# Optimization experiments

Measured on AMD Instinct MI355X. Metric: run time of the kernel, lower is better.

## Reference

```python
import jax, jax.numpy as jnp
import numpy as np

B, T, I, H, O = 8192, 128, 28, 64, 10


def setup_inputs() -> dict:
    key = jax.random.key(0)
    ks = jax.random.split(key, 7)
    s_ih = 1.0 / np.sqrt(H)
    return {
        "x": jax.random.normal(ks[0], (B, T, I), dtype=jnp.float32),
        "W_ih": jax.random.uniform(ks[1], (H, I), minval=-s_ih, maxval=s_ih, dtype=jnp.float32),
        "W_hh": jax.random.uniform(ks[2], (H, H), minval=-s_ih, maxval=s_ih, dtype=jnp.float32),
        "b_ih": jax.random.uniform(ks[3], (H,), minval=-s_ih, maxval=s_ih, dtype=jnp.float32),
        "b_hh": jax.random.uniform(ks[4], (H,), minval=-s_ih, maxval=s_ih, dtype=jnp.float32),
        "W_out": jax.random.uniform(ks[5], (O, H), minval=-1.0 / np.sqrt(H), maxval=1.0 / np.sqrt(H), dtype=jnp.float32),
        "b_out": jax.random.uniform(ks[6], (O,), minval=-1.0 / np.sqrt(H), maxval=1.0 / np.sqrt(H), dtype=jnp.float32),
    }


def reference(x, W_ih, W_hh, b_ih, b_hh, W_out, b_out):
    # Elman RNN: h_t = tanh(x_t @ W_ih^T + b_ih + h_{t-1} @ W_hh^T + b_hh)
    # Precompute the input projection for all timesteps in one big GEMM.
    xproj = jnp.einsum('bti,hi->bth', x, W_ih) + b_ih + b_hh  # [B,T,H]
    h0 = jnp.zeros((x.shape[0], W_hh.shape[0]), dtype=x.dtype)

    def step(h, xp_t):
        h_new = jnp.tanh(xp_t + h @ W_hh.T)
        return h_new, None

    # scan over time axis: move T to leading axis
    h_last, _ = jax.lax.scan(step, h0, jnp.swapaxes(xproj, 0, 1))
    # final linear on last hidden state (r_out[:, -1, :])
    return h_last @ W_out.T + b_out  # [B,O]
```

## Files before the change

### kernel.cpp

```cpp
#include <hip/hip_runtime.h>

#define B_ 8192
#define T_ 128
#define I_ 28
#define H_ 64
#define O_ 10
#define RING 8
#define SLOTF 512
#define HS 72

typedef __attribute__((ext_vector_type(8))) short bf16x8;
typedef __attribute__((ext_vector_type(4))) float f32x4;
typedef __attribute__((ext_vector_type(4))) unsigned int u32x4;

__device__ __forceinline__ unsigned short f2bf(float f) {
    unsigned int u = __builtin_bit_cast(unsigned int, f);
    u += 0x7fffu + ((u >> 16) & 1u);
    return (unsigned short)(u >> 16);
}
__device__ __forceinline__ unsigned int cvtpk(float lo, float hi) {
    unsigned int r;
    asm("v_cvt_pk_bf16_f32 %0, %1, %2" : "=v"(r) : "v"(lo), "v"(hi));
    return r;
}
__device__ __forceinline__ bf16x8 mkfrag(unsigned int a, unsigned int b,
                                         unsigned int c, unsigned int d) {
    u32x4 u = {a, b, c, d};
    return __builtin_bit_cast(bf16x8, u);
}
__device__ __forceinline__ float exp2f_fast(float x) {
#if __has_builtin(__builtin_amdgcn_exp2f)
    return __builtin_amdgcn_exp2f(x);
#else
    return __expf(x * 0.6931471805599453f);
#endif
}
__device__ __forceinline__ unsigned int tanh2_bf(float xa, float xb) {
    float ta = exp2f_fast(xa * 2.885390081777927f);
    float tb = exp2f_fast(xb * 2.885390081777927f);
    float ra = __builtin_amdgcn_rcpf(1.0f + ta);
    float rb = __builtin_amdgcn_rcpf(1.0f + tb);
    return cvtpk(fmaf(-2.0f, ra, 1.0f), fmaf(-2.0f, rb, 1.0f));
}

__device__ __forceinline__ void gload_lds(const float* g, float* l) {
    __builtin_amdgcn_global_load_lds(
        (const __attribute__((address_space(1))) unsigned int*)g,
        (__attribute__((address_space(3))) unsigned int*)l, 16, 0, 0);
}

#define MFMA(A, B, C) __builtin_amdgcn_mfma_f32_16x16x32_bf16((A), (B), (C), 0, 0, 0)

__launch_bounds__(256, 1)
__global__ void rnn_split_kernel(const float* __restrict__ x,
                                 const float* __restrict__ W_ih,
                                 const float* __restrict__ W_hh,
                                 const float* __restrict__ b_ih,
                                 const float* __restrict__ b_hh,
                                 const float* __restrict__ W_out,
                                 const float* __restrict__ b_out,
                                 float* __restrict__ out) {
    __shared__ __align__(16) float xs[RING][SLOTF];
    __shared__ __align__(16) unsigned short hb[2][16 * HS];

    const int tid = threadIdx.x;
    const int lane = tid & 63;
    const int w = tid >> 6;
    const int m = lane & 15;
    const int g = lane >> 4;
    const int b0 = blockIdx.x * 16;
    const int row = b0 + m;

    bf16x8 wih, whhA, whhB;
    f32x4 biasC;
    {
        const int nA = 8 * (m >> 2) + 4 * (w & 1) + (m & 3) + 32 * (w >> 1);
#pragma unroll
        for (int j = 0; j < 8; ++j) {
            const int k = 8 * g + j;
            wih[j]  = (k < I_) ? (short)f2bf(W_ih[nA * I_ + k]) : (short)0;
            whhA[j] = (short)f2bf(W_hh[nA * H_ + k]);
            whhB[j] = (short)f2bf(W_hh[nA * H_ + 32 + k]);
        }
#pragma unroll
        for (int r = 0; r < 4; ++r) {
            const int nb = 8 * g + 4 * (w & 1) + r + 32 * (w >> 1);
            biasC[r] = b_ih[nb] + b_hh[nb];
        }
    }
    const int wbase = m * HS + 8 * g + 4 * (w & 1) + 32 * (w >> 1);
    const int rbase = m * HS + 8 * g;

    const int cA = lane;
    const int cB = (64 + lane <= 111) ? (64 + lane) : 111;
    const float* gA = x + (size_t)(b0 + cA / 7) * (T_ * I_) + (cA % 7) * 4;
    const float* gB = x + (size_t)(b0 + cB / 7) * (T_ * I_) + (cB % 7) * 4;

#define ISSUE(s, tt) do {                                                    \
        const int tc_ = ((tt) < T_) ? (tt) : (T_ - 1);                       \
        gload_lds(gA + (size_t)tc_ * I_, &xs[s][0]);                         \
        gload_lds(gB + (size_t)tc_ * I_, &xs[s][256]);                       \
    } while (0)

    const int xoff = m * 28 + g * 8;
    const int hoff = (g < 3) ? 4 : 0;

#define XFRAG(s, dst) do {                                                   \
        const f32x4 lo_ = *reinterpret_cast<const f32x4*>(&xs[s][xoff]);     \
        const f32x4 hi_ = *reinterpret_cast<const f32x4*>(&xs[s][xoff + hoff]); \
        dst = mkfrag(cvtpk(lo_[0], lo_[1]), cvtpk(lo_[2], lo_[3]),           \
                     cvtpk(hi_[0], hi_[1]), cvtpk(hi_[2], hi_[3]));          \
    } while (0)

    __builtin_amdgcn_sched_barrier(0);
    asm volatile("s_waitcnt vmcnt(0)" ::: "memory");
    __builtin_amdgcn_sched_barrier(0);

    if (w == 0) {
        ISSUE(0, 0); ISSUE(1, 1); ISSUE(2, 2); ISSUE(3, 3);
        ISSUE(4, 4); ISSUE(5, 5); ISSUE(6, 6); ISSUE(7, 7);
        asm volatile("s_waitcnt vmcnt(10)" ::: "memory");
    }
    asm volatile("s_barrier" ::: "memory");

    f32x4 pxA, pxB;
    {
        bf16x8 xf0; XFRAG(0, xf0);
        pxA = MFMA(wih, xf0, biasC);
    }
    bf16x8 h0f = mkfrag(0, 0, 0, 0), h1f = mkfrag(0, 0, 0, 0);

#define STEP(u, TB, PXC, PXN) do {                                            \
        bf16x8 xf; XFRAG(((u) + 1) & 7, xf);                                  \
        PXN = MFMA(wih, xf, biasC);                                           \
        f32x4 aA = MFMA(whhA, h0f, PXC);                                      \
        aA = MFMA(whhB, h1f, aA);                                             \
        const unsigned int p0 = tanh2_bf(aA[0], aA[1]);                       \
        const unsigned int p1 = tanh2_bf(aA[2], aA[3]);                       \
        uint2 pv; pv.x = p0; pv.y = p1;                                       \
        *reinterpret_cast<uint2*>(&hb[((u) + 1) & 1][wbase]) = pv;            \
        if (w == 0) {                                                         \
            ISSUE((u), (TB) + (u) + 8);                                       \
            asm volatile("s_waitcnt vmcnt(10)" ::: "memory");                 \
        }                                                                     \
        asm volatile("s_waitcnt lgkmcnt(0)\n\ts_barrier" ::: "memory");       \
        h0f = *reinterpret_cast<const bf16x8*>(&hb[((u) + 1) & 1][rbase]);    \
        h1f = *reinterpret_cast<const bf16x8*>(&hb[((u) + 1) & 1][rbase + 32]); \
    } while (0)

    for (int tb = 0; tb < T_; tb += 8) {
        STEP(0, tb, pxA, pxB); STEP(1, tb, pxB, pxA);
        STEP(2, tb, pxA, pxB); STEP(3, tb, pxB, pxA);
        STEP(4, tb, pxA, pxB); STEP(5, tb, pxB, pxA);
        STEP(6, tb, pxA, pxB); STEP(7, tb, pxB, pxA);
    }
#undef STEP
#undef XFRAG
#undef ISSUE

    if (w == 0) {
        float hf[16];
        {
            u32x4 H0 = __builtin_bit_cast(u32x4, h0f);
            u32x4 H1 = __builtin_bit_cast(u32x4, h1f);
#pragma unroll
            for (int p = 0; p < 4; ++p) {
                hf[2 * p]     = __builtin_bit_cast(float, H0[p] << 16);
                hf[2 * p + 1] = __builtin_bit_cast(float, H0[p] & 0xffff0000u);
                hf[8 + 2 * p]     = __builtin_bit_cast(float, H1[p] << 16);
                hf[8 + 2 * p + 1] = __builtin_bit_cast(float, H1[p] & 0xffff0000u);
            }
        }
        float pacc[O_];
#pragma unroll
        for (int o = 0; o < O_; ++o) {
            const float* wo = W_out + o * H_;
            float4 wA = *reinterpret_cast<const float4*>(wo + 8 * g);
            float4 wB = *reinterpret_cast<const float4*>(wo + 8 * g + 4);
            float4 wC = *reinterpret_cast<const float4*>(wo + 32 + 8 * g);
            float4 wD = *reinterpret_cast<const float4*>(wo + 32 + 8 * g + 4);
            float s = hf[0] * wA.x + hf[1] * wA.y + hf[2] * wA.z + hf[3] * wA.w
                    + hf[4] * wB.x + hf[5] * wB.y + hf[6] * wB.z + hf[7] * wB.w
                    + hf[8] * wC.x + hf[9] * wC.y + hf[10] * wC.z + hf[11] * wC.w
                    + hf[12] * wD.x + hf[13] * wD.y + hf[14] * wD.z + hf[15] * wD.w;
            s += __shfl_xor(s, 16);
            s += __shfl_xor(s, 32);
            pacc[o] = s;
        }
        if (g == 0) {
#pragma unroll
            for (int o = 0; o < O_; ++o)
                out[(size_t)row * O_ + o] = pacc[o] + b_out[o];
        }
    }
}

extern "C" void kernel_launch(void* const* d_in, const int* in_sizes, int n_in,
                              void* d_out, int out_size, void* d_ws, size_t ws_size,
                              hipStream_t stream) {
    const float* x     = (const float*)d_in[0];
    const float* W_ih  = (const float*)d_in[1];
    const float* W_hh  = (const float*)d_in[2];
    const float* b_ih  = (const float*)d_in[3];
    const float* b_hh  = (const float*)d_in[4];
    const float* W_out = (const float*)d_in[5];
    const float* b_out = (const float*)d_in[6];
    float* out = (float*)d_out;

    dim3 grid(B_ / 16);
    dim3 block(256);
    rnn_split_kernel<<<grid, block, 0, stream>>>(x, W_ih, W_hh, b_ih, b_hh,
                                                 W_out, b_out, out);
}
```

Before: 44.86 us.

## Replace LDS ring of async x loads with per-wave register prefetch

Drops the shared-memory ring that wave 0 filled with global_load_lds, and has every wave load its own x fragment straight from global memory into registers, prefetched four timesteps ahead in rotating register sets. This removes the LDS staging traffic, wave 0's extra issue work and the vmcnt waits inside the barrier-synchronised step. In exchange each of the four waves now loads the same x data redundantly, which multiplies global/L2 request traffic, and load latency must be hidden by the four-step register lookahead rather than the eight-slot ring.

```diff
diff --git a/kernel.cpp b/kernel.cpp
--- a/kernel.cpp
+++ b/kernel.cpp
@@ -5,8 +5,6 @@
 #define I_ 28
 #define H_ 64
 #define O_ 10
-#define RING 8
-#define SLOTF 512
 #define HS 72
 
 typedef __attribute__((ext_vector_type(8))) short bf16x8;
@@ -43,12 +41,6 @@
     return cvtpk(fmaf(-2.0f, ra, 1.0f), fmaf(-2.0f, rb, 1.0f));
 }
 
-__device__ __forceinline__ void gload_lds(const float* g, float* l) {
-    __builtin_amdgcn_global_load_lds(
-        (const __attribute__((address_space(1))) unsigned int*)g,
-        (__attribute__((address_space(3))) unsigned int*)l, 16, 0, 0);
-}
-
 #define MFMA(A, B, C) __builtin_amdgcn_mfma_f32_16x16x32_bf16((A), (B), (C), 0, 0, 0)
 
 __launch_bounds__(256, 1)
@@ -60,7 +52,6 @@
                                  const float* __restrict__ W_out,
                                  const float* __restrict__ b_out,
                                  float* __restrict__ out) {
-    __shared__ __align__(16) float xs[RING][SLOTF];
     __shared__ __align__(16) unsigned short hb[2][16 * HS];
 
     const int tid = threadIdx.x;
@@ -91,72 +82,56 @@
     const int wbase = m * HS + 8 * g + 4 * (w & 1) + 32 * (w >> 1);
     const int rbase = m * HS + 8 * g;
 
-    const int cA = lane;
-    const int cB = (64 + lane <= 111) ? (64 + lane) : 111;
-    const float* gA = x + (size_t)(b0 + cA / 7) * (T_ * I_) + (cA % 7) * 4;
-    const float* gB = x + (size_t)(b0 + cB / 7) * (T_ * I_) + (cB % 7) * 4;
+    const float* xp  = x + (size_t)row * (T_ * I_) + 8 * g;
+    const float* xph = (g < 3) ? (xp + 4) : xp;
 
-#define ISSUE(s, tt) do {                                                    \
+    float4 l0, h0v, l1, h1v, l2, h2v, l3, h3v;
+
+#define LOADX(LO, HI, tt) do {                                               \
         const int tc_ = ((tt) < T_) ? (tt) : (T_ - 1);                       \
-        gload_lds(gA + (size_t)tc_ * I_, &xs[s][0]);                         \
-        gload_lds(gB + (size_t)tc_ * I_, &xs[s][256]);                       \
+        LO = *reinterpret_cast<const float4*>(xp + tc_ * I_);                \
+        HI = *reinterpret_cast<const float4*>(xph + tc_ * I_);               \
     } while (0)
 
-    const int xoff = m * 28 + g * 8;
-    const int hoff = (g < 3) ? 4 : 0;
+#define XF(LO, HI, dst)                                                      \
+    dst = mkfrag(cvtpk(LO.x, LO.y), cvtpk(LO.z, LO.w),                       \
+                 cvtpk(HI.x, HI.y), cvtpk(HI.z, HI.w))
 
-#define XFRAG(s, dst) do {                                                   \
-        const f32x4 lo_ = *reinterpret_cast<const f32x4*>(&xs[s][xoff]);     \
-        const f32x4 hi_ = *reinterpret_cast<const f32x4*>(&xs[s][xoff + hoff]); \
-        dst = mkfrag(cvtpk(lo_[0], lo_[1]), cvtpk(lo_[2], lo_[3]),           \
-                     cvtpk(hi_[0], hi_[1]), cvtpk(hi_[2], hi_[3]));          \
-    } while (0)
-
-    __builtin_amdgcn_sched_barrier(0);
-    asm volatile("s_waitcnt vmcnt(0)" ::: "memory");
-    __builtin_amdgcn_sched_barrier(0);
-
-    if (w == 0) {
-        ISSUE(0, 0); ISSUE(1, 1); ISSUE(2, 2); ISSUE(3, 3);
-        ISSUE(4, 4); ISSUE(5, 5); ISSUE(6, 6); ISSUE(7, 7);
-        asm volatile("s_waitcnt vmcnt(10)" ::: "memory");
-    }
-    asm volatile("s_barrier" ::: "memory");
-
+    LOADX(l0, h0v, 0);
     f32x4 pxA, pxB;
     {
-        bf16x8 xf0; XFRAG(0, xf0);
+        bf16x8 xf0; XF(l0, h0v, xf0);
         pxA = MFMA(wih, xf0, biasC);
     }
+    LOADX(l0, h0v, 4);
+    LOADX(l1, h1v, 1); LOADX(l2, h2v, 2); LOADX(l3, h3v, 3);
+
     bf16x8 h0f = mkfrag(0, 0, 0, 0), h1f = mkfrag(0, 0, 0, 0);
 
-#define STEP(u, TB, PXC, PXN) do {                                            \
-        bf16x8 xf; XFRAG(((u) + 1) & 7, xf);                                  \
+#define STEP(u, TB, PXC, PXN, LO, HI) do {                                    \
+        bf16x8 xf; XF(LO, HI, xf);                                            \
         PXN = MFMA(wih, xf, biasC);                                           \
+        LOADX(LO, HI, (TB) + (u) + 5);                                        \
         f32x4 aA = MFMA(whhA, h0f, PXC);                                      \
         aA = MFMA(whhB, h1f, aA);                                             \
         const unsigned int p0 = tanh2_bf(aA[0], aA[1]);                       \
         const unsigned int p1 = tanh2_bf(aA[2], aA[3]);                       \
         uint2 pv; pv.x = p0; pv.y = p1;                                       \
         *reinterpret_cast<uint2*>(&hb[((u) + 1) & 1][wbase]) = pv;            \
-        if (w == 0) {                                                         \
-            ISSUE((u), (TB) + (u) + 8);                                       \
-            asm volatile("s_waitcnt vmcnt(10)" ::: "memory");                 \
-        }                                                                     \
         asm volatile("s_waitcnt lgkmcnt(0)\n\ts_barrier" ::: "memory");       \
         h0f = *reinterpret_cast<const bf16x8*>(&hb[((u) + 1) & 1][rbase]);    \
         h1f = *reinterpret_cast<const bf16x8*>(&hb[((u) + 1) & 1][rbase + 32]); \
     } while (0)
 
     for (int tb = 0; tb < T_; tb += 8) {
-        STEP(0, tb, pxA, pxB); STEP(1, tb, pxB, pxA);
-        STEP(2, tb, pxA, pxB); STEP(3, tb, pxB, pxA);
-        STEP(4, tb, pxA, pxB); STEP(5, tb, pxB, pxA);
-        STEP(6, tb, pxA, pxB); STEP(7, tb, pxB, pxA);
+        STEP(0, tb, pxA, pxB, l1, h1v); STEP(1, tb, pxB, pxA, l2, h2v);
+        STEP(2, tb, pxA, pxB, l3, h3v); STEP(3, tb, pxB, pxA, l0, h0v);
+        STEP(4, tb, pxA, pxB, l1, h1v); STEP(5, tb, pxB, pxA, l2, h2v);
+        STEP(6, tb, pxA, pxB, l3, h3v); STEP(7, tb, pxB, pxA, l0, h0v);
     }
 #undef STEP
-#undef XFRAG
-#undef ISSUE
+#undef XF
+#undef LOADX
 
     if (w == 0) {
         float hf[16];
```

Result: slower. 68.39 us (+52.5%).

## Halve waves per block, each wave computing two hidden-unit tiles

Applied to the files above, without the earlier changes.

Each block now uses 2 waves instead of 4, with each wave holding weights for two 16-column hidden tiles and issuing twice the MFMA and tanh work per timestep. The hidden-state store becomes a single 16-byte write per lane. This reduces barrier participants and LDS write count per step but lengthens each wave's serial per-step critical path and lowers wave-level parallelism on the CU.

```diff
diff --git a/kernel.cpp b/kernel.cpp
--- a/kernel.cpp
+++ b/kernel.cpp
@@ -51,15 +51,15 @@
 
 #define MFMA(A, B, C) __builtin_amdgcn_mfma_f32_16x16x32_bf16((A), (B), (C), 0, 0, 0)
 
-__launch_bounds__(256, 1)
-__global__ void rnn_split_kernel(const float* __restrict__ x,
-                                 const float* __restrict__ W_ih,
-                                 const float* __restrict__ W_hh,
-                                 const float* __restrict__ b_ih,
-                                 const float* __restrict__ b_hh,
-                                 const float* __restrict__ W_out,
-                                 const float* __restrict__ b_out,
-                                 float* __restrict__ out) {
+__launch_bounds__(128, 1)
+__global__ void rnn_split2_kernel(const float* __restrict__ x,
+                                  const float* __restrict__ W_ih,
+                                  const float* __restrict__ W_hh,
+                                  const float* __restrict__ b_ih,
+                                  const float* __restrict__ b_hh,
+                                  const float* __restrict__ W_out,
+                                  const float* __restrict__ b_out,
+                                  float* __restrict__ out) {
     __shared__ __align__(16) float xs[RING][SLOTF];
     __shared__ __align__(16) unsigned short hb[2][16 * HS];
 
@@ -71,24 +71,30 @@
     const int b0 = blockIdx.x * 16;
     const int row = b0 + m;
 
-    bf16x8 wih, whhA, whhB;
-    f32x4 biasC;
-    {
-        const int nA = 8 * (m >> 2) + 4 * (w & 1) + (m & 3) + 32 * (w >> 1);
+    bf16x8 wih0, wih1, whhA0, whhA1, whhB0, whhB1;
+    f32x4 biasC0, biasC1;
+#pragma unroll
+    for (int tt = 0; tt < 2; ++tt) {
+        const int t = 2 * w + tt;
+        const int nA = 8 * (m >> 2) + 4 * (t & 1) + (m & 3) + 32 * (t >> 1);
+        bf16x8 wi, wa, wb;
 #pragma unroll
         for (int j = 0; j < 8; ++j) {
             const int k = 8 * g + j;
-            wih[j]  = (k < I_) ? (short)f2bf(W_ih[nA * I_ + k]) : (short)0;
-            whhA[j] = (short)f2bf(W_hh[nA * H_ + k]);
-            whhB[j] = (short)f2bf(W_hh[nA * H_ + 32 + k]);
-        }
+            wi[j] = (k < I_) ? (short)f2bf(W_ih[nA * I_ + k]) : (short)0;
+            wa[j] = (short)f2bf(W_hh[nA * H_ + k]);
+            wb[j] = (short)f2bf(W_hh[nA * H_ + 32 + k]);
+        }
+        f32x4 bc;
 #pragma unroll
         for (int r = 0; r < 4; ++r) {
-            const int nb = 8 * g + 4 * (w & 1) + r + 32 * (w >> 1);
-            biasC[r] = b_ih[nb] + b_hh[nb];
-        }
-    }
-    const int wbase = m * HS + 8 * g + 4 * (w & 1) + 32 * (w >> 1);
+            const int nb = 8 * g + 4 * (t & 1) + r + 32 * (t >> 1);
+            bc[r] = b_ih[nb] + b_hh[nb];
+        }
+        if (tt == 0) { wih0 = wi; whhA0 = wa; whhB0 = wb; biasC0 = bc; }
+        else         { wih1 = wi; whhA1 = wa; whhB1 = wb; biasC1 = bc; }
+    }
+    const int wbase = m * HS + 8 * g + 32 * w;
     const int rbase = m * HS + 8 * g;
 
     const int cA = lane;
@@ -123,22 +129,28 @@
     }
     asm volatile("s_barrier" ::: "memory");
 
-    f32x4 pxA, pxB;
+    f32x4 pxA0, pxA1, pxB0, pxB1;
     {
         bf16x8 xf0; XFRAG(0, xf0);
-        pxA = MFMA(wih, xf0, biasC);
+        pxA0 = MFMA(wih0, xf0, biasC0);
+        pxA1 = MFMA(wih1, xf0, biasC1);
     }
     bf16x8 h0f = mkfrag(0, 0, 0, 0), h1f = mkfrag(0, 0, 0, 0);
 
-#define STEP(u, TB, PXC, PXN) do {                                            \
+#define STEP(u, TB, PXC0, PXC1, PXN0, PXN1) do {                              \
         bf16x8 xf; XFRAG(((u) + 1) & 7, xf);                                  \
-        PXN = MFMA(wih, xf, biasC);                                           \
-        f32x4 aA = MFMA(whhA, h0f, PXC);                                      \
-        aA = MFMA(whhB, h1f, aA);                                             \
-        const unsigned int p0 = tanh2_bf(aA[0], aA[1]);                       \
-        const unsigned int p1 = tanh2_bf(aA[2], aA[3]);                       \
-        uint2 pv; pv.x = p0; pv.y = p1;                                       \
-        *reinterpret_cast<uint2*>(&hb[((u) + 1) & 1][wbase]) = pv;            \
+        PXN0 = MFMA(wih0, xf, biasC0);                                        \
+        PXN1 = MFMA(wih1, xf, biasC1);                                        \
+        f32x4 a0 = MFMA(whhA0, h0f, PXC0);                                    \
+        a0 = MFMA(whhB0, h1f, a0);                                            \
+        f32x4 a1 = MFMA(whhA1, h0f, PXC1);                                    \
+        a1 = MFMA(whhB1, h1f, a1);                                            \
+        u32x4 pv;                                                             \
+        pv[0] = tanh2_bf(a0[0], a0[1]);                                       \
+        pv[1] = tanh2_bf(a0[2], a0[3]);                                       \
+        pv[2] = tanh2_bf(a1[0], a1[1]);                                       \
+        pv[3] = tanh2_bf(a1[2], a1[3]);                                       \
+        *reinterpret_cast<u32x4*>(&hb[((u) + 1) & 1][wbase]) = pv;            \
         if (w == 0) {                                                         \
             ISSUE((u), (TB) + (u) + 8);                                       \
             asm volatile("s_waitcnt vmcnt(10)" ::: "memory");                 \
@@ -149,10 +161,10 @@
     } while (0)
 
     for (int tb = 0; tb < T_; tb += 8) {
-        STEP(0, tb, pxA, pxB); STEP(1, tb, pxB, pxA);
-        STEP(2, tb, pxA, pxB); STEP(3, tb, pxB, pxA);
-        STEP(4, tb, pxA, pxB); STEP(5, tb, pxB, pxA);
-        STEP(6, tb, pxA, pxB); STEP(7, tb, pxB, pxA);
+        STEP(0, tb, pxA0, pxA1, pxB0, pxB1); STEP(1, tb, pxB0, pxB1, pxA0, pxA1);
+        STEP(2, tb, pxA0, pxA1, pxB0, pxB1); STEP(3, tb, pxB0, pxB1, pxA0, pxA1);
+        STEP(4, tb, pxA0, pxA1, pxB0, pxB1); STEP(5, tb, pxB0, pxB1, pxA0, pxA1);
+        STEP(6, tb, pxA0, pxA1, pxB0, pxB1); STEP(7, tb, pxB0, pxB1, pxA0, pxA1);
     }
 #undef STEP
 #undef XFRAG
@@ -208,7 +220,7 @@
     float* out = (float*)d_out;
 
     dim3 grid(B_ / 16);
-    dim3 block(256);
-    rnn_split_kernel<<<grid, block, 0, stream>>>(x, W_ih, W_hh, b_ih, b_hh,
-                                                 W_out, b_out, out);
-}
+    dim3 block(128);
+    rnn_split2_kernel<<<grid, block, 0, stream>>>(x, W_ih, W_hh, b_ih, b_hh,
+                                                  W_out, b_out, out);
+}
```

New measurement: 64.98 us. +44.9%, slower.
